# Performance work log

Measured on AMD Instinct MI355X. Metric: run time of the kernel, lower is better.

The kernel has to match this reference:

```python
import jax, jax.numpy as jnp
import numpy as np

PAD = 0  # padding token id; its embedding row is zero (padding_idx)


def setup_inputs() -> dict:
    key = jax.random.key(0)
    k1, k2, k3 = jax.random.split(key, 3)
    HOPS, VOCAB, D = 3, 50257, 128
    B, M, S = 32, 512, 6        # batch, memory slots, tokens per slot
    T, L = 128, 64              # trees per example, tokens per (flattened) tree
    # hop+1 embedding tables, normal(0, 0.1) like the torch init
    C = 0.1 * jax.random.normal(k1, (HOPS + 1, VOCAB, D), dtype=jnp.float32)
    C = C.at[:, PAD].set(0.0)   # padding_idx row = 0
    story = jax.random.randint(k2, (B, M, S), 0, VOCAB, dtype=jnp.int32)
    kb_tokens = jax.random.randint(k3, (B, T, L), 0, VOCAB, dtype=jnp.int32)
    return {"C": C, "story": story, "kb_tokens": kb_tokens}


def reference(C, story, kb_tokens):
    # C: [hops+1, V, D]; story: [B, M, S]; kb_tokens: [B, T, L]
    hops = C.shape[0] - 1
    B = story.shape[0]
    D = C.shape[-1]
    u = jnp.zeros((B, D), dtype=C.dtype)
    for hop in range(hops):
        # key memory: story slots (sum over tokens) + tree memories (sum over
        # all subtree tokens == dfs recursive sum, since PAD embeds to zero)
        m_story_A = jnp.take(C[hop], story, axis=0).sum(axis=2)       # [B,M,D]
        tree_A = jnp.take(C[hop], kb_tokens, axis=0).sum(axis=2)      # [B,T,D]
        m_A = jnp.concatenate([m_story_A, tree_A], axis=1)            # [B,M+T,D]
        prob = jax.nn.softmax(jnp.einsum("bmd,bd->bm", m_A, u), axis=1)
        # value memory with next-hop table
        m_story_C = jnp.take(C[hop + 1], story, axis=0).sum(axis=2)
        tree_C = jnp.take(C[hop + 1], kb_tokens, axis=0).sum(axis=2)
        m_C = jnp.concatenate([m_story_C, tree_C], axis=1)
        o_k = jnp.einsum("bm,bmd->bd", prob, m_C)
        u = u + o_k
    return u
```

## Files before the change

kernel.cpp:

```cpp
#include <hip/hip_runtime.h>
#include <math.h>

constexpr int HOPS  = 3;
constexpr int VOCAB = 50257;
constexpr int DIM   = 128;
constexpr int NB    = 32;
constexpr int NM    = 512;
constexpr int NS    = 6;
constexpr int NT    = 128;
constexpr int NL    = 64;
constexpr int SLOTS = NM + NT;
constexpr size_t TS = (size_t)VOCAB * DIM;
constexpr size_t TABSTRIDE = (size_t)NB * SLOTS * DIM;
constexpr int CHUNKS = SLOTS / 64;

constexpr size_t CH_ELEMS = (size_t)VOCAB * 3 * DIM;
constexpr int NE8 = (int)(CH_ELEMS / 8);

typedef _Float16 half8 __attribute__((ext_vector_type(8)));

constexpr int TREE_BLOCKS  = NB * NT / 16;
constexpr int STORY_BLOCKS = NB * NM / 16;
constexpr int GATHER_BLOCKS = TREE_BLOCKS + STORY_BLOCKS;

__global__ __launch_bounds__(256) void convert_k(
    const float* __restrict__ C, _Float16* __restrict__ Ch)
{
    const int e8 = blockIdx.x * 256 + threadIdx.x;
    if (e8 >= NE8) return;
    const size_t base = (size_t)e8 * 8;
    const size_t v    = base / 384;
    const int    rem  = (int)(base % 384);
    const int    tab  = rem >> 7;
    const int    d    = rem & 127;
    const float* src = C + (size_t)(1 + tab) * TS + v * DIM + d;
    float4 f0 = *(const float4*)(src);
    float4 f1 = *(const float4*)(src + 4);
    half8 h;
    h[0] = (_Float16)f0.x; h[1] = (_Float16)f0.y;
    h[2] = (_Float16)f0.z; h[3] = (_Float16)f0.w;
    h[4] = (_Float16)f1.x; h[5] = (_Float16)f1.y;
    h[6] = (_Float16)f1.z; h[7] = (_Float16)f1.w;
    *(half8*)(Ch + base) = h;
}

__global__ __launch_bounds__(256) void gather_fused(
    const _Float16* __restrict__ Ch, const int* __restrict__ story,
    const int* __restrict__ kb, _Float16* __restrict__ msum)
{
    const int wave = threadIdx.x >> 6, lane = threadIdx.x & 63;
    const int q = lane >> 4, l16 = lane & 15;
    const int qbase = lane & 48;

    float a0[8] = {0,0,0,0,0,0,0,0};
    float a1[8] = {0,0,0,0,0,0,0,0};
    float a2[8] = {0,0,0,0,0,0,0,0};

    const bool is_tree = (blockIdx.x % 5) == 0;
    int b, slot;

    if (is_tree) {
        const int g = (blockIdx.x / 5) * 16 + wave * 4 + q;
        b = g >> 7; slot = NM + (g & (NT - 1));
        const int* idx = kb + (size_t)g * NL;
        #pragma unroll
        for (int o = 0; o < 4; ++o) {
            const int tokv = idx[o * 16 + l16];
            #pragma unroll
            for (int i = 0; i < 16; ++i) {
                const int s = __shfl(tokv, qbase + i);
                const _Float16* p = Ch + (size_t)s * (3 * DIM) + l16 * 8;
                half8 v0 = *(const half8*)(p);
                half8 v1 = *(const half8*)(p + DIM);
                half8 v2 = *(const half8*)(p + 2 * DIM);
                #pragma unroll
                for (int j = 0; j < 8; ++j) {
                    a0[j] += (float)v0[j];
                    a1[j] += (float)v1[j];
                    a2[j] += (float)v2[j];
                }
            }
        }
    } else {
        const int sb = blockIdx.x - blockIdx.x / 5 - 1;
        const int g = sb * 16 + wave * 4 + q;
        b = g >> 9; slot = g & (NM - 1);
        const int* idx = story + (size_t)g * NS;
        const int tokv = (l16 < NS) ? idx[l16] : 0;
        #pragma unroll
        for (int i = 0; i < NS; ++i) {
            const int s = __shfl(tokv, qbase + i);
            const _Float16* p = Ch + (size_t)s * (3 * DIM) + l16 * 8;
            half8 v0 = *(const half8*)(p);
            half8 v1 = *(const half8*)(p + DIM);
            half8 v2 = *(const half8*)(p + 2 * DIM);
            #pragma unroll
            for (int j = 0; j < 8; ++j) {
                a0[j] += (float)v0[j];
                a1[j] += (float)v1[j];
                a2[j] += (float)v2[j];
            }
        }
    }

    const size_t o = ((size_t)b * SLOTS + slot) * DIM + l16 * 8;
    half8 h0, h1, h2;
    #pragma unroll
    for (int j = 0; j < 8; ++j) {
        h0[j] = (_Float16)a0[j]; h1[j] = (_Float16)a1[j]; h2[j] = (_Float16)a2[j];
    }
    *(half8*)(msum + o)                 = h0;
    *(half8*)(msum + o + TABSTRIDE)     = h1;
    *(half8*)(msum + o + 2 * TABSTRIDE) = h2;
}

__global__ __launch_bounds__(256) void hop0_k(
    const _Float16* __restrict__ msum, float* __restrict__ u)
{
    const int b = blockIdx.x, t = threadIdx.x, d = t & (DIM - 1), sub = t >> 7;
    const _Float16* mC = msum + ((size_t)b * SLOTS + sub * (SLOTS / 2)) * DIM + d;
    float acc = 0.f;
    #pragma unroll 16
    for (int m = 0; m < SLOTS / 2; ++m) acc += (float)mC[(size_t)m * DIM];
    __shared__ float red[256];
    red[t] = acc;
    __syncthreads();
    if (t < DIM) u[b * DIM + t] = (red[t] + red[t + 128]) * (1.f / SLOTS);
}

__device__ __forceinline__ float dot128h(const _Float16* __restrict__ row,
                                         const float* __restrict__ u_s)
{
    float acc = 0.f;
    const half8* r8 = (const half8*)row;
    #pragma unroll
    for (int i = 0; i < DIM / 8; ++i) {
        half8 h = r8[i];
        #pragma unroll
        for (int j = 0; j < 8; ++j) acc = fmaf((float)h[j], u_s[8 * i + j], acc);
    }
    return acc;
}

__global__ __launch_bounds__(256) void scores_softmax_k(
    const _Float16* __restrict__ msum, const float* __restrict__ u,
    float* __restrict__ sc, int tab)
{
    const int b = blockIdx.x, t = threadIdx.x, wv = t >> 6, ln = t & 63;
    __shared__ float u_s[DIM];
    __shared__ float red[4];
    if (t < DIM) u_s[t] = u[b * DIM + t];
    __syncthreads();

    const _Float16* mA = msum + (size_t)tab * TABSTRIDE + (size_t)b * SLOTS * DIM;
    float s0 = dot128h(mA + (size_t)t * DIM, u_s);
    float s1 = dot128h(mA + (size_t)(t + 256) * DIM, u_s);
    float s2 = (t < SLOTS - 512) ? dot128h(mA + (size_t)(t + 512) * DIM, u_s)
                                 : -INFINITY;

    float lmax = fmaxf(fmaxf(s0, s1), s2);
    #pragma unroll
    for (int off = 32; off > 0; off >>= 1) lmax = fmaxf(lmax, __shfl_xor(lmax, off));
    if (ln == 0) red[wv] = lmax;
    __syncthreads();
    lmax = fmaxf(fmaxf(red[0], red[1]), fmaxf(red[2], red[3]));
    __syncthreads();

    float e0 = expf(s0 - lmax), e1 = expf(s1 - lmax);
    float e2 = (t < SLOTS - 512) ? expf(s2 - lmax) : 0.f;
    float lsum = e0 + e1 + e2;
    #pragma unroll
    for (int off = 32; off > 0; off >>= 1) lsum += __shfl_xor(lsum, off);
    if (ln == 0) red[wv] = lsum;
    __syncthreads();
    const float inv = 1.0f / (red[0] + red[1] + red[2] + red[3]);

    float* s = sc + b * SLOTS;
    s[t] = e0 * inv;
    s[t + 256] = e1 * inv;
    if (t < SLOTS - 512) s[t + 512] = e2 * inv;
}

__global__ __launch_bounds__(256) void weighted_k(
    const _Float16* __restrict__ msum, const float* __restrict__ probs,
    float* __restrict__ u, int tab)
{
    const int b = blockIdx.x / CHUNKS, chunk = blockIdx.x % CHUNKS;
    const int t = threadIdx.x, d = t & (DIM - 1), sub = t >> 7;
    __shared__ float p[64];
    if (t < 64) p[t] = probs[b * SLOTS + chunk * 64 + t];
    __syncthreads();
    const _Float16* mC = msum + (size_t)tab * TABSTRIDE +
                         ((size_t)b * SLOTS + chunk * 64 + sub * 32) * DIM + d;
    float acc = 0.f;
    #pragma unroll
    for (int m = 0; m < 32; ++m)
        acc = fmaf(p[sub * 32 + m], (float)mC[(size_t)m * DIM], acc);
    __shared__ float red[256];
    red[t] = acc;
    __syncthreads();
    if (t < DIM) atomicAdd(&u[b * DIM + d], red[t] + red[t + 128]);
}

extern "C" void kernel_launch(void* const* d_in, const int* in_sizes, int n_in,
                              void* d_out, int out_size, void* d_ws, size_t ws_size,
                              hipStream_t stream) {
    const float* C     = (const float*)d_in[0];
    const int*   story = (const int*)d_in[1];
    const int*   kb    = (const int*)d_in[2];
    float*       u     = (float*)d_out;

    _Float16* Ch   = (_Float16*)d_ws;
    _Float16* msum = Ch + CH_ELEMS;
    float*    sc   = (float*)(msum + 3 * TABSTRIDE);

    convert_k<<<(NE8 + 255) / 256, 256, 0, stream>>>(C, Ch);
    gather_fused<<<GATHER_BLOCKS, 256, 0, stream>>>(Ch, story, kb, msum);
    hop0_k<<<NB, 256, 0, stream>>>(msum , u);

    for (int hop = 1; hop < HOPS; ++hop) {
        scores_softmax_k<<<NB, 256, 0, stream>>>(msum, u, sc, hop - 1);
        weighted_k<<<NB * CHUNKS, 256, 0, stream>>>(msum, sc, u, hop);
    }
}
```

Before: 221.1 us.

## Overlap table conversion with story gather; one wave per tree with shuffle reduce

Merges the fp16 table conversion and the story-slot gather into one launch. Even blocks convert the table in a grid-stride loop while odd blocks gather story tokens directly from the fp32 tables, so the story path no longer waits on the conversion. The tree gather becomes its own kernel with one wave per tree: each lane quarter sums 16 tokens and the partials are combined by cross-lane shuffles, which spreads the work over more waves. The cost is more fp32 bytes read for story tokens, plus a shuffle reduction and idle lanes on the tree store.

```diff
diff --git a/kernel.cpp b/kernel.cpp
--- a/kernel.cpp
+++ b/kernel.cpp
@@ -18,100 +18,114 @@
 constexpr int NE8 = (int)(CH_ELEMS / 8);
 
 typedef _Float16 half8 __attribute__((ext_vector_type(8)));
-
-constexpr int TREE_BLOCKS  = NB * NT / 16;
-constexpr int STORY_BLOCKS = NB * NM / 16;
-constexpr int GATHER_BLOCKS = TREE_BLOCKS + STORY_BLOCKS;
-
-__global__ __launch_bounds__(256) void convert_k(
-    const float* __restrict__ C, _Float16* __restrict__ Ch)
-{
-    const int e8 = blockIdx.x * 256 + threadIdx.x;
-    if (e8 >= NE8) return;
-    const size_t base = (size_t)e8 * 8;
-    const size_t v    = base / 384;
-    const int    rem  = (int)(base % 384);
-    const int    tab  = rem >> 7;
-    const int    d    = rem & 127;
-    const float* src = C + (size_t)(1 + tab) * TS + v * DIM + d;
-    float4 f0 = *(const float4*)(src);
-    float4 f1 = *(const float4*)(src + 4);
-    half8 h;
-    h[0] = (_Float16)f0.x; h[1] = (_Float16)f0.y;
-    h[2] = (_Float16)f0.z; h[3] = (_Float16)f0.w;
-    h[4] = (_Float16)f1.x; h[5] = (_Float16)f1.y;
-    h[6] = (_Float16)f1.z; h[7] = (_Float16)f1.w;
-    *(half8*)(Ch + base) = h;
-}
-
-__global__ __launch_bounds__(256) void gather_fused(
-    const _Float16* __restrict__ Ch, const int* __restrict__ story,
-    const int* __restrict__ kb, _Float16* __restrict__ msum)
+typedef _Float16 half4 __attribute__((ext_vector_type(4)));
+
+constexpr int CONV_BLOCKS  = 2048;
+constexpr int STORY_BLOCKS = 2048;
+constexpr int K1_BLOCKS    = CONV_BLOCKS + STORY_BLOCKS;
+constexpr int TREE_BLOCKS  = NB * NT / 4;
+
+__device__ __forceinline__ void addf4(float4& a, const float4& v) {
+    a.x += v.x; a.y += v.y; a.z += v.z; a.w += v.w;
+}
+
+__global__ __launch_bounds__(256) void convert_story_k(
+    const float* __restrict__ C, const int* __restrict__ story,
+    _Float16* __restrict__ Ch, _Float16* __restrict__ msum)
+{
+    if (blockIdx.x & 1) {
+        const int sb   = blockIdx.x >> 1;
+        const int wave = threadIdx.x >> 6, lane = threadIdx.x & 63;
+        const int h = lane >> 5, l32 = lane & 31;
+        const int g = sb * 8 + wave * 2 + h;
+        const int b = g >> 9, slot = g & (NM - 1);
+
+        const int* idx = story + (size_t)g * NS;
+        const int tokv = (l32 < NS) ? idx[l32] : 0;
+
+        const float* Cb = C + TS + (size_t)l32 * 4;
+        float4 a0 = {0,0,0,0}, a1 = {0,0,0,0}, a2 = {0,0,0,0};
+        #pragma unroll
+        for (int i = 0; i < NS; ++i) {
+            const int s = __shfl(tokv, h * 32 + i);
+            const float* p = Cb + (size_t)s * DIM;
+            addf4(a0, *(const float4*)(p));
+            addf4(a1, *(const float4*)(p + TS));
+            addf4(a2, *(const float4*)(p + 2 * TS));
+        }
+        half4 h0, h1, h2;
+        h0[0]=(_Float16)a0.x; h0[1]=(_Float16)a0.y; h0[2]=(_Float16)a0.z; h0[3]=(_Float16)a0.w;
+        h1[0]=(_Float16)a1.x; h1[1]=(_Float16)a1.y; h1[2]=(_Float16)a1.z; h1[3]=(_Float16)a1.w;
+        h2[0]=(_Float16)a2.x; h2[1]=(_Float16)a2.y; h2[2]=(_Float16)a2.z; h2[3]=(_Float16)a2.w;
+        const size_t o = ((size_t)b * SLOTS + slot) * DIM + l32 * 4;
+        *(half4*)(msum + o)                 = h0;
+        *(half4*)(msum + o + TABSTRIDE)     = h1;
+        *(half4*)(msum + o + 2 * TABSTRIDE) = h2;
+    } else {
+        const int cb = blockIdx.x >> 1;
+        for (int e8 = cb * 256 + threadIdx.x; e8 < NE8; e8 += CONV_BLOCKS * 256) {
+            const size_t base = (size_t)e8 * 8;
+            const size_t v    = base / 384;
+            const int    rem  = (int)(base % 384);
+            const int    tab  = rem >> 7;
+            const int    d    = rem & 127;
+            const float* src = C + (size_t)(1 + tab) * TS + v * DIM + d;
+            float4 f0 = *(const float4*)(src);
+            float4 f1 = *(const float4*)(src + 4);
+            half8 h;
+            h[0]=(_Float16)f0.x; h[1]=(_Float16)f0.y; h[2]=(_Float16)f0.z; h[3]=(_Float16)f0.w;
+            h[4]=(_Float16)f1.x; h[5]=(_Float16)f1.y; h[6]=(_Float16)f1.z; h[7]=(_Float16)f1.w;
+            *(half8*)(Ch + base) = h;
+        }
+    }
+}
+
+__global__ __launch_bounds__(256) void tree_gather(
+    const _Float16* __restrict__ Ch, const int* __restrict__ kb,
+    _Float16* __restrict__ msum)
 {
     const int wave = threadIdx.x >> 6, lane = threadIdx.x & 63;
     const int q = lane >> 4, l16 = lane & 15;
-    const int qbase = lane & 48;
+    const int g = blockIdx.x * 4 + wave;
+    const int b = g >> 7, tr = g & (NT - 1);
+
+    const int tok = kb[(size_t)g * NL + lane];
 
     float a0[8] = {0,0,0,0,0,0,0,0};
     float a1[8] = {0,0,0,0,0,0,0,0};
     float a2[8] = {0,0,0,0,0,0,0,0};
 
-    const bool is_tree = (blockIdx.x % 5) == 0;
-    int b, slot;
-
-    if (is_tree) {
-        const int g = (blockIdx.x / 5) * 16 + wave * 4 + q;
-        b = g >> 7; slot = NM + (g & (NT - 1));
-        const int* idx = kb + (size_t)g * NL;
-        #pragma unroll
-        for (int o = 0; o < 4; ++o) {
-            const int tokv = idx[o * 16 + l16];
-            #pragma unroll
-            for (int i = 0; i < 16; ++i) {
-                const int s = __shfl(tokv, qbase + i);
-                const _Float16* p = Ch + (size_t)s * (3 * DIM) + l16 * 8;
-                half8 v0 = *(const half8*)(p);
-                half8 v1 = *(const half8*)(p + DIM);
-                half8 v2 = *(const half8*)(p + 2 * DIM);
-                #pragma unroll
-                for (int j = 0; j < 8; ++j) {
-                    a0[j] += (float)v0[j];
-                    a1[j] += (float)v1[j];
-                    a2[j] += (float)v2[j];
-                }
-            }
-        }
-    } else {
-        const int sb = blockIdx.x - blockIdx.x / 5 - 1;
-        const int g = sb * 16 + wave * 4 + q;
-        b = g >> 9; slot = g & (NM - 1);
-        const int* idx = story + (size_t)g * NS;
-        const int tokv = (l16 < NS) ? idx[l16] : 0;
-        #pragma unroll
-        for (int i = 0; i < NS; ++i) {
-            const int s = __shfl(tokv, qbase + i);
-            const _Float16* p = Ch + (size_t)s * (3 * DIM) + l16 * 8;
-            half8 v0 = *(const half8*)(p);
-            half8 v1 = *(const half8*)(p + DIM);
-            half8 v2 = *(const half8*)(p + 2 * DIM);
-            #pragma unroll
-            for (int j = 0; j < 8; ++j) {
-                a0[j] += (float)v0[j];
-                a1[j] += (float)v1[j];
-                a2[j] += (float)v2[j];
-            }
-        }
-    }
-
-    const size_t o = ((size_t)b * SLOTS + slot) * DIM + l16 * 8;
-    half8 h0, h1, h2;
+    #pragma unroll
+    for (int i = 0; i < 16; ++i) {
+        const int s = __shfl(tok, (lane & 48) + i);
+        const _Float16* p = Ch + (size_t)s * (3 * DIM) + l16 * 8;
+        half8 v0 = *(const half8*)(p);
+        half8 v1 = *(const half8*)(p + DIM);
+        half8 v2 = *(const half8*)(p + 2 * DIM);
+        #pragma unroll
+        for (int j = 0; j < 8; ++j) {
+            a0[j] += (float)v0[j];
+            a1[j] += (float)v1[j];
+            a2[j] += (float)v2[j];
+        }
+    }
     #pragma unroll
     for (int j = 0; j < 8; ++j) {
-        h0[j] = (_Float16)a0[j]; h1[j] = (_Float16)a1[j]; h2[j] = (_Float16)a2[j];
-    }
-    *(half8*)(msum + o)                 = h0;
-    *(half8*)(msum + o + TABSTRIDE)     = h1;
-    *(half8*)(msum + o + 2 * TABSTRIDE) = h2;
+        a0[j] += __shfl_xor(a0[j], 16); a0[j] += __shfl_xor(a0[j], 32);
+        a1[j] += __shfl_xor(a1[j], 16); a1[j] += __shfl_xor(a1[j], 32);
+        a2[j] += __shfl_xor(a2[j], 16); a2[j] += __shfl_xor(a2[j], 32);
+    }
+    if (q == 0) {
+        half8 h0, h1, h2;
+        #pragma unroll
+        for (int j = 0; j < 8; ++j) {
+            h0[j] = (_Float16)a0[j]; h1[j] = (_Float16)a1[j]; h2[j] = (_Float16)a2[j];
+        }
+        const size_t o = ((size_t)b * SLOTS + NM + tr) * DIM + l16 * 8;
+        *(half8*)(msum + o)                 = h0;
+        *(half8*)(msum + o + TABSTRIDE)     = h1;
+        *(half8*)(msum + o + 2 * TABSTRIDE) = h2;
+    }
 }
 
 __global__ __launch_bounds__(256) void hop0_k(
@@ -214,8 +228,8 @@
     _Float16* msum = Ch + CH_ELEMS;
     float*    sc   = (float*)(msum + 3 * TABSTRIDE);
 
-    convert_k<<<(NE8 + 255) / 256, 256, 0, stream>>>(C, Ch);
-    gather_fused<<<GATHER_BLOCKS, 256, 0, stream>>>(Ch, story, kb, msum);
+    convert_story_k<<<K1_BLOCKS, 256, 0, stream>>>(C, story, Ch, msum);
+    tree_gather<<<TREE_BLOCKS, 256, 0, stream>>>(Ch, kb, msum);
     hop0_k<<<NB, 256, 0, stream>>>(msum , u);
 
     for (int hop = 1; hop < HOPS; ++hop) {
```

After: 221.6 us. About the same (+0.2%).
